# Optimization experiments

Measured on AMD Instinct MI355X. Metric: run time of the kernel, lower is better.

The kernel has to match this reference:

```python
import jax, jax.numpy as jnp
import numpy as np

N_NODES = 50000   # batch_size * n_verts
N_EDGES = 800000
D_FEAT = 128
UNITS = 256


def setup_inputs() -> dict:
    key = jax.random.key(0)
    k1, k2, k3, k4, k5 = jax.random.split(key, 5)
    features = jax.random.normal(k1, (N_NODES, D_FEAT), dtype=jnp.float32)
    edge_row = jax.random.randint(k2, (N_EDGES,), 0, N_NODES, dtype=jnp.int32)
    edge_col = jax.random.randint(k3, (N_EDGES,), 0, N_NODES, dtype=jnp.int32)
    edge_val = jax.random.uniform(k4, (N_EDGES,), dtype=jnp.float32)
    W = jax.random.normal(k5, (D_FEAT, UNITS), dtype=jnp.float32) * (1.0 / np.sqrt(D_FEAT))
    return {"features": features, "edge_row": edge_row, "edge_col": edge_col,
            "edge_val": edge_val, "W": W}


def reference(features, edge_row, edge_col, edge_val, W):
    # features: [N, F] (already the (batch*n_verts, F) layout the layer reshapes to)
    # A in COO: A[edge_row[e], edge_col[e]] = edge_val[e]
    n = features.shape[0]
    # in_degree = row-sum of A values, +1 for self loop
    in_degree = jax.ops.segment_sum(edge_val, edge_row, num_segments=n) + 1.0
    invsqrt_deg = jax.lax.rsqrt(in_degree)                       # [N]
    normalized = invsqrt_deg[:, None] * features                 # [N, F]
    # pooled = A @ normalized  (gather source rows, scale, scatter-add to dest)
    msgs = edge_val[:, None] * normalized[edge_col]              # [E, F]
    pooled = jax.ops.segment_sum(msgs, edge_row, num_segments=n) # [N, F]
    # self-loop contribution (normalized case)
    pooled = pooled + invsqrt_deg[:, None] * normalized
    # dense projection + relu
    out = jax.nn.relu(pooled @ W)                                # [N, units]
    return out
```

## Files before the change

kernel.cpp:

```cpp
#include <hip/hip_runtime.h>

constexpr int N = 50000;
constexpr int E = 800000;
constexpr int F = 128;
constexpr int U = 256;

constexpr int R    = 8;
constexpr int NK   = N * R;
constexpr int EBLK = E / 256;
constexpr int SBLK = (NK + 255) / 256;
constexpr int CH   = (SBLK + 255) / 256;

typedef __attribute__((ext_vector_type(8))) short short8;
typedef __attribute__((ext_vector_type(4))) float float4v;

__device__ inline unsigned short f32_to_bf16(float x) {
    unsigned int u = __float_as_uint(x);
    unsigned int r = (u + 0x7fffu + ((u >> 16) & 1u)) >> 16;
    return (unsigned short)r;
}
__device__ inline float bf_lo(unsigned int u) { return __uint_as_float(u << 16); }
__device__ inline float bf_hi(unsigned int u) { return __uint_as_float(u & 0xffff0000u); }

__global__ __launch_bounds__(256) void hist_kernel(const int* __restrict__ erow,
                                                   int* __restrict__ cnt,
                                                   unsigned int* __restrict__ rankp,
                                                   const float* __restrict__ W,
                                                   unsigned short* __restrict__ Wt) {
    if (blockIdx.x >= EBLK) {
        int idx = (blockIdx.x - EBLK) * 256 + threadIdx.x;
        int k = idx >> 8;
        int n = idx & 255;
        Wt[n * F + k] = f32_to_bf16(W[idx]);
        return;
    }
    int e = blockIdx.x * 256 + threadIdx.x;
    int key = erow[e] * R + (blockIdx.x & (R - 1));
    int rk = atomicAdd(&cnt[key], 1);
    rankp[e] = ((unsigned int)key << 12) | (unsigned int)rk;
}

__global__ __launch_bounds__(256) void blksum_kernel(const int* __restrict__ cnt,
                                                     int* __restrict__ blk_sum) {
    int i = blockIdx.x * 256 + threadIdx.x;
    int v = (i < NK) ? cnt[i] : 0;
    #pragma unroll
    for (int off = 32; off > 0; off >>= 1) v += __shfl_down(v, off, 64);
    __shared__ int s[4];
    if ((threadIdx.x & 63) == 0) s[threadIdx.x >> 6] = v;
    __syncthreads();
    if (threadIdx.x == 0) blk_sum[blockIdx.x] = s[0] + s[1] + s[2] + s[3];
}

__global__ __launch_bounds__(256) void scansum_kernel(const int* __restrict__ blk_sum,
                                                      int* __restrict__ blk_off,
                                                      int* __restrict__ rp2) {
    __shared__ int sh[256];
    int t = threadIdx.x;
    int loc[CH];
    int s = 0;
    #pragma unroll
    for (int i = 0; i < CH; ++i) {
        int idx = t * CH + i;
        int v = (idx < SBLK) ? blk_sum[idx] : 0;
        loc[i] = v;
        s += v;
    }
    sh[t] = s;
    __syncthreads();
    for (int off = 1; off < 256; off <<= 1) {
        int u = (t >= off) ? sh[t - off] : 0;
        __syncthreads();
        sh[t] += u;
        __syncthreads();
    }
    int run = sh[t] - s;
    #pragma unroll
    for (int i = 0; i < CH; ++i) {
        int idx = t * CH + i;
        if (idx < SBLK) {
            blk_off[idx] = run;
            run += loc[i];
        }
    }
    if (t == 0) rp2[NK] = E;
}

__global__ __launch_bounds__(256) void blkscan_kernel(const int* __restrict__ cnt,
                                                      const int* __restrict__ blk_off,
                                                      int* __restrict__ rp2) {
    __shared__ int sh[256];
    int t = threadIdx.x;
    int i = blockIdx.x * 256 + t;
    int v = (i < NK) ? cnt[i] : 0;
    sh[t] = v;
    __syncthreads();
    for (int off = 1; off < 256; off <<= 1) {
        int u = (t >= off) ? sh[t - off] : 0;
        __syncthreads();
        sh[t] += u;
        __syncthreads();
    }
    if (i < NK) rp2[i] = blk_off[blockIdx.x] + sh[t] - v;
}

__global__ __launch_bounds__(256) void permute_kernel(const int* __restrict__ ecol,
                                                      const float* __restrict__ eval,
                                                      const unsigned int* __restrict__ rankp,
                                                      const int* __restrict__ rp2,
                                                      int2* __restrict__ csr) {
    int e = blockIdx.x * 256 + threadIdx.x;
    if (e < E) {
        unsigned int pk = rankp[e];
        int p = rp2[pk >> 12] + (int)(pk & 0xFFFu);
        csr[p] = make_int2(ecol[e], __float_as_int(eval[e]));
    }
}

__global__ __launch_bounds__(256) void norm_kernel(const float* __restrict__ feat,
                                                   const int* __restrict__ rp2,
                                                   const int2* __restrict__ csr,
                                                   float* __restrict__ iv,
                                                   unsigned int* __restrict__ nrm) {
    int gtid = blockIdx.x * 256 + threadIdx.x;
    int n    = gtid >> 6;
    int lane = threadIdx.x & 63;
    if (n >= N) return;

    int e0 = rp2[n * R], e1 = rp2[n * R + R];
    float s = 0.f;
    for (int e = e0 + lane; e < e1; e += 64) s += __int_as_float(csr[e].y);
    #pragma unroll
    for (int off = 32; off > 0; off >>= 1) s += __shfl_xor(s, off, 64);
    float iv_ = rsqrtf(s + 1.0f);
    if (lane == 0) iv[n] = iv_;

    float2 f = ((const float2*)feat)[n * 64 + lane];
    nrm[n * 64 + lane] =
        (unsigned int)f32_to_bf16(iv_ * f.x) | ((unsigned int)f32_to_bf16(iv_ * f.y) << 16);
}

__global__ __launch_bounds__(256) void gather_kernel(const int* __restrict__ rp2,
                                                     const int2* __restrict__ csr,
                                                     const unsigned int* __restrict__ nrm,
                                                     const float* __restrict__ iv,
                                                     unsigned int* __restrict__ pooledb) {
    int gtid = blockIdx.x * 256 + threadIdx.x;
    int n    = gtid >> 6;
    int lane = threadIdx.x & 63;
    if (n >= N) return;

    float iv_ = iv[n];
    unsigned int self = nrm[n * 64 + lane];
    float acc0 = iv_ * bf_lo(self);
    float acc1 = iv_ * bf_hi(self);

    int e = rp2[n * R], e1 = rp2[n * R + R];
    for (; e + 7 < e1; e += 8) {
        int2 p0 = csr[e],     p1 = csr[e + 1], p2 = csr[e + 2], p3 = csr[e + 3];
        int2 p4 = csr[e + 4], p5 = csr[e + 5], p6 = csr[e + 6], p7 = csr[e + 7];
        unsigned int u0 = nrm[(size_t)p0.x * 64 + lane];
        unsigned int u1 = nrm[(size_t)p1.x * 64 + lane];
        unsigned int u2 = nrm[(size_t)p2.x * 64 + lane];
        unsigned int u3 = nrm[(size_t)p3.x * 64 + lane];
        unsigned int u4 = nrm[(size_t)p4.x * 64 + lane];
        unsigned int u5 = nrm[(size_t)p5.x * 64 + lane];
        unsigned int u6 = nrm[(size_t)p6.x * 64 + lane];
        unsigned int u7 = nrm[(size_t)p7.x * 64 + lane];
        acc0 += __int_as_float(p0.y) * bf_lo(u0); acc1 += __int_as_float(p0.y) * bf_hi(u0);
        acc0 += __int_as_float(p1.y) * bf_lo(u1); acc1 += __int_as_float(p1.y) * bf_hi(u1);
        acc0 += __int_as_float(p2.y) * bf_lo(u2); acc1 += __int_as_float(p2.y) * bf_hi(u2);
        acc0 += __int_as_float(p3.y) * bf_lo(u3); acc1 += __int_as_float(p3.y) * bf_hi(u3);
        acc0 += __int_as_float(p4.y) * bf_lo(u4); acc1 += __int_as_float(p4.y) * bf_hi(u4);
        acc0 += __int_as_float(p5.y) * bf_lo(u5); acc1 += __int_as_float(p5.y) * bf_hi(u5);
        acc0 += __int_as_float(p6.y) * bf_lo(u6); acc1 += __int_as_float(p6.y) * bf_hi(u6);
        acc0 += __int_as_float(p7.y) * bf_lo(u7); acc1 += __int_as_float(p7.y) * bf_hi(u7);
    }
    for (; e + 3 < e1; e += 4) {
        int2 p0 = csr[e], p1 = csr[e + 1], p2 = csr[e + 2], p3 = csr[e + 3];
        unsigned int u0 = nrm[(size_t)p0.x * 64 + lane];
        unsigned int u1 = nrm[(size_t)p1.x * 64 + lane];
        unsigned int u2 = nrm[(size_t)p2.x * 64 + lane];
        unsigned int u3 = nrm[(size_t)p3.x * 64 + lane];
        acc0 += __int_as_float(p0.y) * bf_lo(u0); acc1 += __int_as_float(p0.y) * bf_hi(u0);
        acc0 += __int_as_float(p1.y) * bf_lo(u1); acc1 += __int_as_float(p1.y) * bf_hi(u1);
        acc0 += __int_as_float(p2.y) * bf_lo(u2); acc1 += __int_as_float(p2.y) * bf_hi(u2);
        acc0 += __int_as_float(p3.y) * bf_lo(u3); acc1 += __int_as_float(p3.y) * bf_hi(u3);
    }
    for (; e < e1; ++e) {
        int2 p0 = csr[e];
        unsigned int u0 = nrm[(size_t)p0.x * 64 + lane];
        acc0 += __int_as_float(p0.y) * bf_lo(u0);
        acc1 += __int_as_float(p0.y) * bf_hi(u0);
    }
    pooledb[n * 64 + lane] =
        (unsigned int)f32_to_bf16(acc0) | ((unsigned int)f32_to_bf16(acc1) << 16);
}

__global__ __launch_bounds__(256) void gemm_mfma_kernel(const unsigned short* __restrict__ Ab,
                                                        const unsigned short* __restrict__ Wt,
                                                        float* __restrict__ out) {
    __shared__ unsigned short As[16384];
    __shared__ unsigned short Bs[16384];
    const int tid = threadIdx.x;
    const int m0 = blockIdx.x * 128;
    const int n0 = blockIdx.y * 128;

    {
        const int r = tid >> 1;
        const int h = tid & 1;
        const int grow = m0 + r;
        const uint4* asrc = (grow < N) ? (const uint4*)(Ab + (size_t)grow * F) : nullptr;
        const uint4* bsrc = (const uint4*)(Wt + (size_t)(n0 + r) * F);
        #pragma unroll
        for (int j = 0; j < 8; ++j) {
            int o = h * 8 + j;
            int ks = o >> 2, quad = o & 3;
            int slot = ((ks * 8 + (r >> 4)) * 64) + (quad << 4) + (r & 15);
            uint4 av = asrc ? asrc[o] : make_uint4(0u, 0u, 0u, 0u);
            ((uint4*)As)[slot] = av;
            ((uint4*)Bs)[slot] = bsrc[o];
        }
    }
    __syncthreads();

    const int wave = tid >> 6;
    const int lane = tid & 63;
    float4v acc[8][2];
    #pragma unroll
    for (int i = 0; i < 8; ++i) {
        acc[i][0] = (float4v){0.f, 0.f, 0.f, 0.f};
        acc[i][1] = (float4v){0.f, 0.f, 0.f, 0.f};
    }

    #pragma unroll
    for (int ks = 0; ks < 4; ++ks) {
        short8 b0 = *(const short8*)&Bs[(((ks * 8 + wave * 2 + 0) * 64) + lane) * 8];
        short8 b1 = *(const short8*)&Bs[(((ks * 8 + wave * 2 + 1) * 64) + lane) * 8];
        #pragma unroll
        for (int mt = 0; mt < 8; ++mt) {
            short8 a = *(const short8*)&As[(((ks * 8 + mt) * 64) + lane) * 8];
            acc[mt][0] = __builtin_amdgcn_mfma_f32_16x16x32_bf16(a, b0, acc[mt][0], 0, 0, 0);
            acc[mt][1] = __builtin_amdgcn_mfma_f32_16x16x32_bf16(a, b1, acc[mt][1], 0, 0, 0);
        }
    }

    const int quad = lane >> 4;
    const int colt = lane & 15;
    #pragma unroll
    for (int mt = 0; mt < 8; ++mt) {
        #pragma unroll
        for (int nt = 0; nt < 2; ++nt) {
            int col = n0 + (wave * 2 + nt) * 16 + colt;
            #pragma unroll
            for (int i = 0; i < 4; ++i) {
                int row = m0 + mt * 16 + quad * 4 + i;
                if (row < N) out[(size_t)row * U + col] = fmaxf(acc[mt][nt][i], 0.f);
            }
        }
    }
}

extern "C" void kernel_launch(void* const* d_in, const int* in_sizes, int n_in,
                              void* d_out, int out_size, void* d_ws, size_t ws_size,
                              hipStream_t stream) {
    (void)in_sizes; (void)n_in; (void)out_size; (void)ws_size;

    const float* feat = (const float*)d_in[0];
    const int*   erow = (const int*)d_in[1];
    const int*   ecol = (const int*)d_in[2];
    const float* eval = (const float*)d_in[3];
    const float* W    = (const float*)d_in[4];
    float* out = (float*)d_out;

    char* ws = (char*)d_ws;
    int*            cnt     = (int*)  (ws + 0);
    int*            rp2     = (int*)  (ws + 1600000);
    int*            blk_sum = (int*)  (ws + 3200064);
    int*            blk_off = (int*)  (ws + 3206336);
    unsigned int*   rankp   = (unsigned int*)(ws + 3212608);
    int2*           csr     = (int2*) (ws + 6412608);
    float*          iv      = (float*)(ws + 12812608);
    unsigned short* Wt      = (unsigned short*)(ws + 13012608);
    unsigned int*   nrm     = (unsigned int*)  (ws + 13078144);
    unsigned int*   pooledb = (unsigned int*)  (ws + 25878144);

    (void)hipMemsetAsync(cnt, 0, (size_t)NK * sizeof(int), stream);

    hist_kernel<<<EBLK + (F * U) / 256, 256, 0, stream>>>(erow, cnt, rankp, W, Wt);

    blksum_kernel <<<SBLK, 256, 0, stream>>>(cnt, blk_sum);
    scansum_kernel<<<1,    256, 0, stream>>>(blk_sum, blk_off, rp2);
    blkscan_kernel<<<SBLK, 256, 0, stream>>>(cnt, blk_off, rp2);

    permute_kernel<<<EBLK, 256, 0, stream>>>(ecol, eval, rankp, rp2, csr);
    norm_kernel  <<<(N * 64) / 256, 256, 0, stream>>>(feat, rp2, csr, iv, nrm);
    gather_kernel<<<(N * 64) / 256, 256, 0, stream>>>(rp2, csr, nrm, iv, pooledb);

    dim3 ggrid((N + 127) / 128, U / 128);
    gemm_mfma_kernel<<<ggrid, 256, 0, stream>>>((const unsigned short*)pooledb, Wt, out);
}
```

Baseline: 213.6 us.

## Pack edge count and fixed-point degree into one 64-bit atomic, drop scan kernel

The histogram kernel now does one 64-bit atomic per edge that adds 1 to a high count field and the edge value as 26-bit fixed point to a low field. The norm kernel then reads the degree directly from four packed slots instead of walking the CSR edges. The single-block scansum kernel is removed; each scan block instead sums the preceding block totals itself. The replication factor R drops from 8 to 4, which halves the packed array but raises atomic contention per slot. Degrees now carry fixed-point rounding error, and each scan block redundantly reads up to about 800 block sums.

```diff
diff --git a/kernel.cpp b/kernel.cpp
--- a/kernel.cpp
+++ b/kernel.cpp
@@ -5,14 +5,17 @@
 constexpr int F = 128;
 constexpr int U = 256;
 
-constexpr int R    = 8;
+constexpr int R    = 4;
 constexpr int NK   = N * R;
 constexpr int EBLK = E / 256;
 constexpr int SBLK = (NK + 255) / 256;
-constexpr int CH   = (SBLK + 255) / 256;
 
 typedef __attribute__((ext_vector_type(8))) short short8;
 typedef __attribute__((ext_vector_type(4))) float float4v;
+
+constexpr float FIXED_SCALE = 67108864.0f;
+constexpr float FIXED_INV   = 1.4901161193847656e-8f;
+constexpr unsigned long long VAL_MASK = 0xFFFFFFFFFFull;
 
 __device__ inline unsigned short f32_to_bf16(float x) {
     unsigned int u = __float_as_uint(x);
@@ -23,7 +26,8 @@
 __device__ inline float bf_hi(unsigned int u) { return __uint_as_float(u & 0xffff0000u); }
 
 __global__ __launch_bounds__(256) void hist_kernel(const int* __restrict__ erow,
-                                                   int* __restrict__ cnt,
+                                                   const float* __restrict__ eval,
+                                                   unsigned long long* __restrict__ packed,
                                                    unsigned int* __restrict__ rankp,
                                                    const float* __restrict__ W,
                                                    unsigned short* __restrict__ Wt) {
@@ -36,14 +40,16 @@
     }
     int e = blockIdx.x * 256 + threadIdx.x;
     int key = erow[e] * R + (blockIdx.x & (R - 1));
-    int rk = atomicAdd(&cnt[key], 1);
-    rankp[e] = ((unsigned int)key << 12) | (unsigned int)rk;
-}
-
-__global__ __launch_bounds__(256) void blksum_kernel(const int* __restrict__ cnt,
+    unsigned long long add =
+        (1ull << 40) | (unsigned long long)(eval[e] * FIXED_SCALE);
+    unsigned long long old = atomicAdd(&packed[key], add);
+    rankp[e] = ((unsigned int)key << 12) | (unsigned int)(old >> 40);
+}
+
+__global__ __launch_bounds__(256) void blksum_kernel(const unsigned long long* __restrict__ packed,
                                                      int* __restrict__ blk_sum) {
     int i = blockIdx.x * 256 + threadIdx.x;
-    int v = (i < NK) ? cnt[i] : 0;
+    int v = (i < NK) ? (int)(packed[i] >> 40) : 0;
     #pragma unroll
     for (int off = 32; off > 0; off >>= 1) v += __shfl_down(v, off, 64);
     __shared__ int s[4];
@@ -52,21 +58,26 @@
     if (threadIdx.x == 0) blk_sum[blockIdx.x] = s[0] + s[1] + s[2] + s[3];
 }
 
-__global__ __launch_bounds__(256) void scansum_kernel(const int* __restrict__ blk_sum,
-                                                      int* __restrict__ blk_off,
+__global__ __launch_bounds__(256) void blkscan_kernel(const unsigned long long* __restrict__ packed,
+                                                      const int* __restrict__ blk_sum,
                                                       int* __restrict__ rp2) {
     __shared__ int sh[256];
+    __shared__ int waves[4];
+    __shared__ int base_sh;
     int t = threadIdx.x;
-    int loc[CH];
-    int s = 0;
-    #pragma unroll
-    for (int i = 0; i < CH; ++i) {
-        int idx = t * CH + i;
-        int v = (idx < SBLK) ? blk_sum[idx] : 0;
-        loc[i] = v;
-        s += v;
-    }
-    sh[t] = s;
+    int bid = blockIdx.x;
+
+    int pre = 0;
+    for (int idx = t; idx < bid; idx += 256) pre += blk_sum[idx];
+    #pragma unroll
+    for (int off = 32; off > 0; off >>= 1) pre += __shfl_down(pre, off, 64);
+    if ((t & 63) == 0) waves[t >> 6] = pre;
+    __syncthreads();
+    if (t == 0) base_sh = waves[0] + waves[1] + waves[2] + waves[3];
+
+    int i = bid * 256 + t;
+    int v = (i < NK) ? (int)(packed[i] >> 40) : 0;
+    sh[t] = v;
     __syncthreads();
     for (int off = 1; off < 256; off <<= 1) {
         int u = (t >= off) ? sh[t - off] : 0;
@@ -74,34 +85,8 @@
         sh[t] += u;
         __syncthreads();
     }
-    int run = sh[t] - s;
-    #pragma unroll
-    for (int i = 0; i < CH; ++i) {
-        int idx = t * CH + i;
-        if (idx < SBLK) {
-            blk_off[idx] = run;
-            run += loc[i];
-        }
-    }
-    if (t == 0) rp2[NK] = E;
-}
-
-__global__ __launch_bounds__(256) void blkscan_kernel(const int* __restrict__ cnt,
-                                                      const int* __restrict__ blk_off,
-                                                      int* __restrict__ rp2) {
-    __shared__ int sh[256];
-    int t = threadIdx.x;
-    int i = blockIdx.x * 256 + t;
-    int v = (i < NK) ? cnt[i] : 0;
-    sh[t] = v;
-    __syncthreads();
-    for (int off = 1; off < 256; off <<= 1) {
-        int u = (t >= off) ? sh[t - off] : 0;
-        __syncthreads();
-        sh[t] += u;
-        __syncthreads();
-    }
-    if (i < NK) rp2[i] = blk_off[blockIdx.x] + sh[t] - v;
+    if (i < NK) rp2[i] = base_sh + sh[t] - v;
+    if (bid == 0 && t == 0) rp2[NK] = E;
 }
 
 __global__ __launch_bounds__(256) void permute_kernel(const int* __restrict__ ecol,
@@ -118,8 +103,7 @@
 }
 
 __global__ __launch_bounds__(256) void norm_kernel(const float* __restrict__ feat,
-                                                   const int* __restrict__ rp2,
-                                                   const int2* __restrict__ csr,
+                                                   const unsigned long long* __restrict__ packed,
                                                    float* __restrict__ iv,
                                                    unsigned int* __restrict__ nrm) {
     int gtid = blockIdx.x * 256 + threadIdx.x;
@@ -127,12 +111,10 @@
     int lane = threadIdx.x & 63;
     if (n >= N) return;
 
-    int e0 = rp2[n * R], e1 = rp2[n * R + R];
-    float s = 0.f;
-    for (int e = e0 + lane; e < e1; e += 64) s += __int_as_float(csr[e].y);
-    #pragma unroll
-    for (int off = 32; off > 0; off >>= 1) s += __shfl_xor(s, off, 64);
-    float iv_ = rsqrtf(s + 1.0f);
+    int kb = n * R;
+    unsigned long long s = (packed[kb] & VAL_MASK) + (packed[kb + 1] & VAL_MASK) +
+                           (packed[kb + 2] & VAL_MASK) + (packed[kb + 3] & VAL_MASK);
+    float iv_ = rsqrtf((float)s * FIXED_INV + 1.0f);
     if (lane == 0) iv[n] = iv_;
 
     float2 f = ((const float2*)feat)[n * 64 + lane];
@@ -274,27 +256,25 @@
     float* out = (float*)d_out;
 
     char* ws = (char*)d_ws;
-    int*            cnt     = (int*)  (ws + 0);
-    int*            rp2     = (int*)  (ws + 1600000);
-    int*            blk_sum = (int*)  (ws + 3200064);
-    int*            blk_off = (int*)  (ws + 3206336);
-    unsigned int*   rankp   = (unsigned int*)(ws + 3212608);
-    int2*           csr     = (int2*) (ws + 6412608);
-    float*          iv      = (float*)(ws + 12812608);
-    unsigned short* Wt      = (unsigned short*)(ws + 13012608);
-    unsigned int*   nrm     = (unsigned int*)  (ws + 13078144);
-    unsigned int*   pooledb = (unsigned int*)  (ws + 25878144);
-
-    (void)hipMemsetAsync(cnt, 0, (size_t)NK * sizeof(int), stream);
-
-    hist_kernel<<<EBLK + (F * U) / 256, 256, 0, stream>>>(erow, cnt, rankp, W, Wt);
-
-    blksum_kernel <<<SBLK, 256, 0, stream>>>(cnt, blk_sum);
-    scansum_kernel<<<1,    256, 0, stream>>>(blk_sum, blk_off, rp2);
-    blkscan_kernel<<<SBLK, 256, 0, stream>>>(cnt, blk_off, rp2);
+    unsigned long long* packed = (unsigned long long*)(ws + 0);
+    int*            blk_sum = (int*)(ws + 1600000);
+    int*            rp2     = (int*)(ws + 1603200);
+    unsigned int*   rankp   = (unsigned int*)(ws + 2403264);
+    int2*           csr     = (int2*)(ws + 5603264);
+    float*          iv      = (float*)(ws + 12003264);
+    unsigned short* Wt      = (unsigned short*)(ws + 12203264);
+    unsigned int*   nrm     = (unsigned int*)(ws + 12268800);
+    unsigned int*   pooledb = (unsigned int*)(ws + 25068800);
+
+    (void)hipMemsetAsync(packed, 0, (size_t)NK * 8, stream);
+
+    hist_kernel<<<EBLK + (F * U) / 256, 256, 0, stream>>>(erow, eval, packed, rankp, W, Wt);
+
+    blksum_kernel<<<SBLK, 256, 0, stream>>>(packed, blk_sum);
+    blkscan_kernel<<<SBLK, 256, 0, stream>>>(packed, blk_sum, rp2);
 
     permute_kernel<<<EBLK, 256, 0, stream>>>(ecol, eval, rankp, rp2, csr);
-    norm_kernel  <<<(N * 64) / 256, 256, 0, stream>>>(feat, rp2, csr, iv, nrm);
+    norm_kernel  <<<(N * 64) / 256, 256, 0, stream>>>(feat, packed, iv, nrm);
     gather_kernel<<<(N * 64) / 256, 256, 0, stream>>>(rp2, csr, nrm, iv, pooledb);
 
     dim3 ggrid((N + 127) / 128, U / 128);
```

Result: slower. 220.0 us (+3.0%).
